# Performance work log

Measured on AMD Instinct MI355X. Metric: run time of the kernel, lower is better.

The kernel has to match this reference:

```python
import jax, jax.numpy as jnp
from jax import lax
import numpy as np

VOCAB, EMBED, HIDDEN, MEL = 256, 256, 1024, 80


def lstm_seq(x_seq, Wih, Whh, bih, bhh):
    """x_seq: [T, B, in]; returns hidden sequence [T, B, H]. PyTorch gate order i,f,g,o."""
    H = Whh.shape[1]
    B = x_seq.shape[1]
    b = bih + bhh

    def step(carry, x):
        h, c = carry
        g = x @ Wih.T + h @ Whh.T + b  # [B, 4H]
        i, f, gg, o = jnp.split(g, 4, axis=-1)
        c = jax.nn.sigmoid(f) * c + jax.nn.sigmoid(i) * jnp.tanh(gg)
        h = jax.nn.sigmoid(o) * jnp.tanh(c)
        return (h, c), h

    init = (jnp.zeros((B, H), x_seq.dtype), jnp.zeros((B, H), x_seq.dtype))
    _, ys = lax.scan(step, init, x_seq)
    return ys


def setup_inputs() -> dict:
    key = jax.random.key(0)
    ks = jax.random.split(key, 13)
    s_h = 1.0 / np.sqrt(HIDDEN)
    u = lambda k, shape, s: jax.random.uniform(k, shape, jnp.float32, -s, s)
    return {
        "text": jax.random.randint(ks[0], (64, 1024), 0, VOCAB),
        "text_lens": jax.random.randint(ks[1], (64,), 1, 1024),
        "max_audio_len": 1000,
        "W_emb": jax.random.normal(ks[2], (VOCAB, EMBED), jnp.float32),
        "enc_Wih": u(ks[3], (4 * HIDDEN, EMBED), s_h),
        "enc_Whh": u(ks[4], (4 * HIDDEN, HIDDEN), s_h),
        "enc_bih": u(ks[5], (4 * HIDDEN,), s_h),
        "enc_bhh": u(ks[6], (4 * HIDDEN,), s_h),
        "dec_Wih": u(ks[7], (4 * HIDDEN, MEL), s_h),
        "dec_Whh": u(ks[8], (4 * HIDDEN, HIDDEN), s_h),
        "dec_bih": u(ks[9], (4 * HIDDEN,), s_h),
        "dec_bhh": u(ks[10], (4 * HIDDEN,), s_h),
        "lin_W": u(ks[11], (MEL, HIDDEN), s_h),
        "lin_b": u(ks[12], (MEL,), s_h),
    }


def reference(text, text_lens, max_audio_len, W_emb, enc_Wih, enc_Whh, enc_bih,
              enc_bhh, dec_Wih, dec_Whh, dec_bih, dec_bhh, lin_W, lin_b):
    B = text.shape[0]
    # Encoder over text (output unused downstream, but computed as in the original).
    emb = W_emb[text]                      # [B, T, E]
    enc_out = lstm_seq(emb.transpose(1, 0, 2), enc_Wih, enc_Whh, enc_bih, enc_bhh)
    enc_out = enc_out.transpose(1, 0, 2)   # [B, T, H]

    b_dec = dec_bih + dec_bhh

    def dec_step(carry, _):
        h, c, x = carry                    # x: [B, MEL] previous frame
        g = x @ dec_Wih.T + h @ dec_Whh.T + b_dec
        i, f, gg, o = jnp.split(g, 4, axis=-1)
        c = jax.nn.sigmoid(f) * c + jax.nn.sigmoid(i) * jnp.tanh(gg)
        h = jax.nn.sigmoid(o) * jnp.tanh(c)
        frame = h @ lin_W.T + lin_b        # [B, MEL]
        return (h, c, frame), frame

    init = (jnp.zeros((B, HIDDEN), jnp.float32),
            jnp.zeros((B, HIDDEN), jnp.float32),
            jnp.zeros((B, MEL), jnp.float32))
    _, frames = lax.scan(dec_step, init, None, length=max_audio_len)
    return frames.transpose(1, 0, 2)       # [B, max_audio_len, MEL]
```

## Files before the change

kernel.cpp:

```cpp
#include <hip/hip_runtime.h>
#include <math.h>

#define HIDDEN 1024
#define MEL    80
#define TSTEPS 1000
#define BATCH  64

#define NBLK 64
#define TPB  1024

typedef unsigned long long ull;

__device__ __forceinline__ float sigm_f(float x) { return 1.0f / (1.0f + __expf(-x)); }
__device__ __forceinline__ float tanh_f(float x) { return 1.0f - 2.0f / (1.0f + __expf(2.0f * x)); }

__global__ __launch_bounds__(TPB, 4) void tts_recur(
    const float* __restrict__ dec_Wih,
    const float* __restrict__ dec_Whh,
    const float* __restrict__ dec_bih,
    const float* __restrict__ dec_bhh,
    const float* __restrict__ lin_W,
    const float* __restrict__ lin_b,
    float* __restrict__ h_hist,
    ull* __restrict__ hbuf)
{
    const int tid  = threadIdx.x;
    const int blk  = blockIdx.x;
    const int wv   = tid >> 6;
    const int lane = tid & 63;
    const int jj   = lane & 15;
    const int gate = lane >> 4;
    const int unit_g = blk * 16 + jj;
    const int row_g  = gate * HIDDEN + unit_g;

    if (wv == 0) __builtin_amdgcn_s_setprio(3);

    __shared__ __align__(16) float hEx[16][64];
    __shared__ float part[2][64 * 17];

    const float* wih = dec_Wih + (size_t)row_g * MEL;
    const float* whh = dec_Whh + (size_t)row_g * HIDDEN + wv * 64;
    float4 w[16];
#pragma unroll
    for (int k = 0; k < 16; ++k)
        w[k] = *(const float4*)(whh + k * 4);
#pragma unroll 1
    for (int m = 0; m < MEL; ++m) {
        const float aw = wih[m];
        const float4* lw4 = (const float4*)(lin_W + (size_t)m * HIDDEN + wv * 64);
#pragma unroll
        for (int k = 0; k < 8; ++k) {
            const float4 lw = lw4[k];
            w[k].x = fmaf(aw, lw.x, w[k].x); w[k].y = fmaf(aw, lw.y, w[k].y);
            w[k].z = fmaf(aw, lw.z, w[k].z); w[k].w = fmaf(aw, lw.w, w[k].w);
        }
#pragma unroll
        for (int k = 8; k < 16; ++k) {
            const float4 lw = lw4[k];
            w[k].x = fmaf(aw, lw.x, w[k].x); w[k].y = fmaf(aw, lw.y, w[k].y);
            w[k].z = fmaf(aw, lw.z, w[k].z); w[k].w = fmaf(aw, lw.w, w[k].w);
        }
    }
    float b_comb_r = dec_bih[row_g] + dec_bhh[row_g];
    const float b_dec_r = b_comb_r;
    for (int m = 0; m < MEL; ++m)
        b_comb_r = fmaf(wih[m], lin_b[m], b_comb_r);

    float c_prev = 0.0f;

    if (wv == 0) {
        const float g = b_dec_r;
        const float gi = __shfl(g, jj, 64);
        const float gg = __shfl(g, 32 + jj, 64);
        const float go = __shfl(g, 48 + jj, 64);
        const float c  = sigm_f(gi) * tanh_f(gg);
        const float h  = sigm_f(go) * tanh_f(c);
        c_prev = c;
        if (lane < 16) {
            const ull pk = ((ull)1u << 32) | (ull)__float_as_uint(h);
            __hip_atomic_store(hbuf + unit_g, pk,
                               __ATOMIC_RELAXED, __HIP_MEMORY_SCOPE_SYSTEM);
            h_hist[unit_g] = h;
        }
    }

    for (int t = 1; t < TSTEPS; ++t) {
        const int buf = t & 1;
        {
            const ull* src = hbuf + ((t - 1) & 1) * HIDDEN;
            ull v = __hip_atomic_load(src + tid, __ATOMIC_RELAXED, __HIP_MEMORY_SCOPE_SYSTEM);
            while ((unsigned)(v >> 32) != (unsigned)t)
                v = __hip_atomic_load(src + tid, __ATOMIC_RELAXED, __HIP_MEMORY_SCOPE_SYSTEM);
            hEx[wv][lane] = __uint_as_float((unsigned)v);
        }
        __builtin_amdgcn_wave_barrier();

        const float4* hp = (const float4*)&hEx[wv][0];
        float a0 = 0.f, a1 = 0.f, a2 = 0.f, a3 = 0.f;
#pragma unroll
        for (int k = 0; k < 16; k += 4) {
            const float4 h0 = hp[k], h1 = hp[k + 1], h2 = hp[k + 2], h3 = hp[k + 3];
            a0 = fmaf(w[k].x, h0.x, a0);   a0 = fmaf(w[k].y, h0.y, a0);
            a0 = fmaf(w[k].z, h0.z, a0);   a0 = fmaf(w[k].w, h0.w, a0);
            a1 = fmaf(w[k+1].x, h1.x, a1); a1 = fmaf(w[k+1].y, h1.y, a1);
            a1 = fmaf(w[k+1].z, h1.z, a1); a1 = fmaf(w[k+1].w, h1.w, a1);
            a2 = fmaf(w[k+2].x, h2.x, a2); a2 = fmaf(w[k+2].y, h2.y, a2);
            a2 = fmaf(w[k+2].z, h2.z, a2); a2 = fmaf(w[k+2].w, h2.w, a2);
            a3 = fmaf(w[k+3].x, h3.x, a3); a3 = fmaf(w[k+3].y, h3.y, a3);
            a3 = fmaf(w[k+3].z, h3.z, a3); a3 = fmaf(w[k+3].w, h3.w, a3);
        }
        part[buf][lane * 17 + wv] = (a0 + a1) + (a2 + a3);
        __syncthreads();

        if (wv == 0) {
            const float* pr = &part[buf][lane * 17];
            float p[16];
#pragma unroll
            for (int i = 0; i < 16; ++i) p[i] = pr[i];
            const float s = (((p[0]+p[1])+(p[2]+p[3])) + ((p[4]+p[5])+(p[6]+p[7])))
                          + (((p[8]+p[9])+(p[10]+p[11])) + ((p[12]+p[13])+(p[14]+p[15])));
            const float g = s + b_comb_r;
            const float gi = __shfl(g, jj, 64);
            const float gf = __shfl(g, 16 + jj, 64);
            const float gg = __shfl(g, 32 + jj, 64);
            const float go = __shfl(g, 48 + jj, 64);
            const float c  = sigm_f(gf) * c_prev + sigm_f(gi) * tanh_f(gg);
            const float h  = sigm_f(go) * tanh_f(c);
            c_prev = c;
            if (lane < 16) {
                const ull pk = ((ull)(unsigned)(t + 1) << 32) | (ull)__float_as_uint(h);
                __hip_atomic_store(hbuf + buf * HIDDEN + unit_g, pk,
                                   __ATOMIC_RELAXED, __HIP_MEMORY_SCOPE_SYSTEM);
                h_hist[(size_t)t * HIDDEN + unit_g] = h;
            }
        }
    }
}

__global__ __launch_bounds__(128) void tts_frames(
    const float* __restrict__ lin_W, const float* __restrict__ lin_b,
    const float* __restrict__ h_hist, float* __restrict__ out)
{
    const int t = blockIdx.x;
    const int tid = threadIdx.x;
    __shared__ __align__(16) float h_sh[HIDDEN];
    __shared__ float f_s[MEL];
    const float4* src = (const float4*)(h_hist + (size_t)t * HIDDEN);
    ((float4*)h_sh)[tid] = src[tid];
    ((float4*)h_sh)[tid + 128] = src[tid + 128];
    __syncthreads();
    if (tid < MEL) {
        const float* wrow = lin_W + (size_t)tid * HIDDEN;
        float acc = lin_b[tid];
#pragma unroll 8
        for (int c = 0; c < HIDDEN; ++c)
            acc = fmaf(wrow[c], h_sh[c], acc);
        f_s[tid] = acc;
    }
    __syncthreads();
    for (int idx = tid; idx < BATCH * MEL; idx += 128) {
        const int b = idx / MEL;
        const int m = idx - b * MEL;
        out[(size_t)b * TSTEPS * MEL + (size_t)t * MEL + m] = f_s[m];
    }
}

extern "C" void kernel_launch(void* const* d_in, const int* in_sizes, int n_in,
                              void* d_out, int out_size, void* d_ws, size_t ws_size,
                              hipStream_t stream) {
    const float* dec_Wih = (const float*)d_in[8];
    const float* dec_Whh = (const float*)d_in[9];
    const float* dec_bih = (const float*)d_in[10];
    const float* dec_bhh = (const float*)d_in[11];
    const float* lin_W   = (const float*)d_in[12];
    const float* lin_b   = (const float*)d_in[13];
    float* out = (float*)d_out;

    float* h_hist = (float*)d_ws;
    ull* hbuf = (ull*)((char*)d_ws + (size_t)TSTEPS * HIDDEN * sizeof(float));

    hipLaunchKernelGGL(tts_recur, dim3(NBLK), dim3(TPB), 0, stream,
                       dec_Wih, dec_Whh, dec_bih, dec_bhh, lin_W, lin_b, h_hist, hbuf);
    hipLaunchKernelGGL(tts_frames, dim3(TSTEPS), dim3(128), 0, stream,
                       lin_W, lin_b, h_hist, out);
}
```

Baseline: 2.187 ms.

## Map one hidden unit per wave to drop block barrier in LSTM recurrence

The persistent recurrent kernel is reorganized so that each wave owns one hidden unit, with its 64 lanes covering 4 gates times 16 column chunks. The cross-wave shared-memory partial sum and __syncthreads are replaced by a shuffle-xor reduction inside the wave. Every wave now reads the full h vector itself, issuing 16 tagged atomic loads per lane into padded LDS. The grid changes to 256 blocks of 256 threads, and atomic scope is narrowed from system to agent. The aim is to remove block-level synchronization and the serial reduction on the per-step critical path, at the cost of 4x more global polling traffic per step.

Measured after the change: 8.702 ms. +297.9%, slower.

```diff
diff --git a/kernel.cpp b/kernel.cpp
--- a/kernel.cpp
+++ b/kernel.cpp
@@ -6,15 +6,17 @@
 #define TSTEPS 1000
 #define BATCH  64
 
-#define NBLK 64
-#define TPB  1024
+#define NBLK 256
+#define TPB  256
 
 typedef unsigned long long ull;
 
 __device__ __forceinline__ float sigm_f(float x) { return 1.0f / (1.0f + __expf(-x)); }
 __device__ __forceinline__ float tanh_f(float x) { return 1.0f - 2.0f / (1.0f + __expf(2.0f * x)); }
 
-__global__ __launch_bounds__(TPB, 4) void tts_recur(
+#define HEXP 1088
+
+__global__ __launch_bounds__(TPB, 1) void tts_recur(
     const float* __restrict__ dec_Wih,
     const float* __restrict__ dec_Whh,
     const float* __restrict__ dec_bih,
@@ -25,21 +27,17 @@
     ull* __restrict__ hbuf)
 {
     const int tid  = threadIdx.x;
-    const int blk  = blockIdx.x;
     const int wv   = tid >> 6;
     const int lane = tid & 63;
-    const int jj   = lane & 15;
     const int gate = lane >> 4;
-    const int unit_g = blk * 16 + jj;
-    const int row_g  = gate * HIDDEN + unit_g;
+    const int c    = lane & 15;
+    const int u    = blockIdx.x * 4 + wv;
+    const int row_g = gate * HIDDEN + u;
 
-    if (wv == 0) __builtin_amdgcn_s_setprio(3);
-
-    __shared__ __align__(16) float hEx[16][64];
-    __shared__ float part[2][64 * 17];
+    __shared__ __align__(16) float hEx[4][HEXP];
 
     const float* wih = dec_Wih + (size_t)row_g * MEL;
-    const float* whh = dec_Whh + (size_t)row_g * HIDDEN + wv * 64;
+    const float* whh = dec_Whh + (size_t)row_g * HIDDEN + c * 64;
     float4 w[16];
 #pragma unroll
     for (int k = 0; k < 16; ++k)
@@ -47,7 +45,7 @@
 #pragma unroll 1
     for (int m = 0; m < MEL; ++m) {
         const float aw = wih[m];
-        const float4* lw4 = (const float4*)(lin_W + (size_t)m * HIDDEN + wv * 64);
+        const float4* lw4 = (const float4*)(lin_W + (size_t)m * HIDDEN + c * 64);
 #pragma unroll
         for (int k = 0; k < 8; ++k) {
             const float4 lw = lw4[k];
@@ -68,34 +66,43 @@
 
     float c_prev = 0.0f;
 
-    if (wv == 0) {
+    {
         const float g = b_dec_r;
-        const float gi = __shfl(g, jj, 64);
-        const float gg = __shfl(g, 32 + jj, 64);
-        const float go = __shfl(g, 48 + jj, 64);
-        const float c  = sigm_f(gi) * tanh_f(gg);
-        const float h  = sigm_f(go) * tanh_f(c);
-        c_prev = c;
-        if (lane < 16) {
+        const float gi = __shfl(g, c, 64);
+        const float gf = __shfl(g, 16 + c, 64);
+        const float gg = __shfl(g, 32 + c, 64);
+        const float go = __shfl(g, 48 + c, 64);
+        const float cc = sigm_f(gf) * c_prev + sigm_f(gi) * tanh_f(gg);
+        const float h  = sigm_f(go) * tanh_f(cc);
+        c_prev = cc;
+        if (lane == 0) {
             const ull pk = ((ull)1u << 32) | (ull)__float_as_uint(h);
-            __hip_atomic_store(hbuf + unit_g, pk,
-                               __ATOMIC_RELAXED, __HIP_MEMORY_SCOPE_SYSTEM);
-            h_hist[unit_g] = h;
+            __hip_atomic_store(hbuf + u, pk,
+                               __ATOMIC_RELAXED, __HIP_MEMORY_SCOPE_AGENT);
+            h_hist[u] = h;
         }
     }
 
     for (int t = 1; t < TSTEPS; ++t) {
-        const int buf = t & 1;
+        const unsigned tag = (unsigned)t;
         {
             const ull* src = hbuf + ((t - 1) & 1) * HIDDEN;
-            ull v = __hip_atomic_load(src + tid, __ATOMIC_RELAXED, __HIP_MEMORY_SCOPE_SYSTEM);
-            while ((unsigned)(v >> 32) != (unsigned)t)
-                v = __hip_atomic_load(src + tid, __ATOMIC_RELAXED, __HIP_MEMORY_SCOPE_SYSTEM);
-            hEx[wv][lane] = __uint_as_float((unsigned)v);
+            ull v[16];
+#pragma unroll
+            for (int j = 0; j < 16; ++j)
+                v[j] = __hip_atomic_load(src + lane + 64 * j,
+                                         __ATOMIC_RELAXED, __HIP_MEMORY_SCOPE_AGENT);
+#pragma unroll
+            for (int j = 0; j < 16; ++j) {
+                while ((unsigned)(v[j] >> 32) != tag)
+                    v[j] = __hip_atomic_load(src + lane + 64 * j,
+                                             __ATOMIC_RELAXED, __HIP_MEMORY_SCOPE_AGENT);
+                hEx[wv][lane + 68 * j] = __uint_as_float((unsigned)v[j]);
+            }
         }
         __builtin_amdgcn_wave_barrier();
 
-        const float4* hp = (const float4*)&hEx[wv][0];
+        const float4* hp = (const float4*)(&hEx[wv][68 * c]);
         float a0 = 0.f, a1 = 0.f, a2 = 0.f, a3 = 0.f;
 #pragma unroll
         for (int k = 0; k < 16; k += 4) {
@@ -109,30 +116,25 @@
             a3 = fmaf(w[k+3].x, h3.x, a3); a3 = fmaf(w[k+3].y, h3.y, a3);
             a3 = fmaf(w[k+3].z, h3.z, a3); a3 = fmaf(w[k+3].w, h3.w, a3);
         }
-        part[buf][lane * 17 + wv] = (a0 + a1) + (a2 + a3);
-        __syncthreads();
+        float acc = (a0 + a1) + (a2 + a3);
+        acc += __shfl_xor(acc, 1, 64);
+        acc += __shfl_xor(acc, 2, 64);
+        acc += __shfl_xor(acc, 4, 64);
+        acc += __shfl_xor(acc, 8, 64);
+        const float g = acc + b_comb_r;
+        const float gi = __shfl(g, c, 64);
+        const float gf = __shfl(g, 16 + c, 64);
+        const float gg = __shfl(g, 32 + c, 64);
+        const float go = __shfl(g, 48 + c, 64);
+        const float cc = sigm_f(gf) * c_prev + sigm_f(gi) * tanh_f(gg);
+        const float h  = sigm_f(go) * tanh_f(cc);
+        c_prev = cc;
 
-        if (wv == 0) {
-            const float* pr = &part[buf][lane * 17];
-            float p[16];
-#pragma unroll
-            for (int i = 0; i < 16; ++i) p[i] = pr[i];
-            const float s = (((p[0]+p[1])+(p[2]+p[3])) + ((p[4]+p[5])+(p[6]+p[7])))
-                          + (((p[8]+p[9])+(p[10]+p[11])) + ((p[12]+p[13])+(p[14]+p[15])));
-            const float g = s + b_comb_r;
-            const float gi = __shfl(g, jj, 64);
-            const float gf = __shfl(g, 16 + jj, 64);
-            const float gg = __shfl(g, 32 + jj, 64);
-            const float go = __shfl(g, 48 + jj, 64);
-            const float c  = sigm_f(gf) * c_prev + sigm_f(gi) * tanh_f(gg);
-            const float h  = sigm_f(go) * tanh_f(c);
-            c_prev = c;
-            if (lane < 16) {
-                const ull pk = ((ull)(unsigned)(t + 1) << 32) | (ull)__float_as_uint(h);
-                __hip_atomic_store(hbuf + buf * HIDDEN + unit_g, pk,
-                                   __ATOMIC_RELAXED, __HIP_MEMORY_SCOPE_SYSTEM);
-                h_hist[(size_t)t * HIDDEN + unit_g] = h;
-            }
+        if (lane == 0) {
+            const ull pk = ((ull)(unsigned)(t + 1) << 32) | (ull)__float_as_uint(h);
+            __hip_atomic_store(hbuf + (t & 1) * HIDDEN + u, pk,
+                               __ATOMIC_RELAXED, __HIP_MEMORY_SCOPE_AGENT);
+            h_hist[(size_t)t * HIDDEN + u] = h;
         }
     }
 }
@@ -153,8 +155,8 @@
         const float* wrow = lin_W + (size_t)tid * HIDDEN;
         float acc = lin_b[tid];
 #pragma unroll 8
-        for (int c = 0; c < HIDDEN; ++c)
-            acc = fmaf(wrow[c], h_sh[c], acc);
+        for (int cc = 0; cc < HIDDEN; ++cc)
+            acc = fmaf(wrow[cc], h_sh[cc], acc);
         f_s[tid] = acc;
     }
     __syncthreads();
```

## Spread LSTM cell update across all waves and use agent-scope atomics

Applied to the files above, without the earlier changes.

The per-step gate reduction and cell update move from wave 0 alone to all 16 waves. Each wave reads 16 partials for its own hidden unit, reduces them with xor shuffles, and computes the cell for that one unit. Inter-block h exchange now uses agent-scope atomics instead of system scope, and the wave-0 priority boost is removed. This aims to cut the serial tail on the recurrence critical path and lower atomic coherence cost. In exchange every wave does redundant transcendental work, and the reduction order changes slightly.

After: 3.874 ms. 77.1% more time.

```diff
diff --git a/kernel.cpp b/kernel.cpp
--- a/kernel.cpp
+++ b/kernel.cpp
@@ -30,10 +30,7 @@
     const int lane = tid & 63;
     const int jj   = lane & 15;
     const int gate = lane >> 4;
-    const int unit_g = blk * 16 + jj;
-    const int row_g  = gate * HIDDEN + unit_g;
-
-    if (wv == 0) __builtin_amdgcn_s_setprio(3);
+    const int row_g  = gate * HIDDEN + blk * 16 + jj;
 
     __shared__ __align__(16) float hEx[16][64];
     __shared__ float part[2][64 * 17];
@@ -66,21 +63,21 @@
     for (int m = 0; m < MEL; ++m)
         b_comb_r = fmaf(wih[m], lin_b[m], b_comb_r);
 
-    float c_prev = 0.0f;
+    float c_prev;
 
-    if (wv == 0) {
-        const float g = b_dec_r;
-        const float gi = __shfl(g, jj, 64);
-        const float gg = __shfl(g, 32 + jj, 64);
-        const float go = __shfl(g, 48 + jj, 64);
+    {
+        const float bdw = __shfl(b_dec_r, (lane & 48) + wv, 64);
+        const float gi = __shfl(bdw, 0, 64);
+        const float gg = __shfl(bdw, 32, 64);
+        const float go = __shfl(bdw, 48, 64);
         const float c  = sigm_f(gi) * tanh_f(gg);
         const float h  = sigm_f(go) * tanh_f(c);
         c_prev = c;
-        if (lane < 16) {
+        if (lane == 0) {
             const ull pk = ((ull)1u << 32) | (ull)__float_as_uint(h);
-            __hip_atomic_store(hbuf + unit_g, pk,
-                               __ATOMIC_RELAXED, __HIP_MEMORY_SCOPE_SYSTEM);
-            h_hist[unit_g] = h;
+            __hip_atomic_store(hbuf + blk * 16 + wv, pk,
+                               __ATOMIC_RELAXED, __HIP_MEMORY_SCOPE_AGENT);
+            h_hist[blk * 16 + wv] = h;
         }
     }
 
@@ -88,9 +85,9 @@
         const int buf = t & 1;
         {
             const ull* src = hbuf + ((t - 1) & 1) * HIDDEN;
-            ull v = __hip_atomic_load(src + tid, __ATOMIC_RELAXED, __HIP_MEMORY_SCOPE_SYSTEM);
+            ull v = __hip_atomic_load(src + tid, __ATOMIC_RELAXED, __HIP_MEMORY_SCOPE_AGENT);
             while ((unsigned)(v >> 32) != (unsigned)t)
-                v = __hip_atomic_load(src + tid, __ATOMIC_RELAXED, __HIP_MEMORY_SCOPE_SYSTEM);
+                v = __hip_atomic_load(src + tid, __ATOMIC_RELAXED, __HIP_MEMORY_SCOPE_AGENT);
             hEx[wv][lane] = __uint_as_float((unsigned)v);
         }
         __builtin_amdgcn_wave_barrier();
@@ -112,26 +109,25 @@
         part[buf][lane * 17 + wv] = (a0 + a1) + (a2 + a3);
         __syncthreads();
 
-        if (wv == 0) {
-            const float* pr = &part[buf][lane * 17];
-            float p[16];
-#pragma unroll
-            for (int i = 0; i < 16; ++i) p[i] = pr[i];
-            const float s = (((p[0]+p[1])+(p[2]+p[3])) + ((p[4]+p[5])+(p[6]+p[7])))
-                          + (((p[8]+p[9])+(p[10]+p[11])) + ((p[12]+p[13])+(p[14]+p[15])));
-            const float g = s + b_comb_r;
-            const float gi = __shfl(g, jj, 64);
-            const float gf = __shfl(g, 16 + jj, 64);
-            const float gg = __shfl(g, 32 + jj, 64);
-            const float go = __shfl(g, 48 + jj, 64);
+        {
+            float s = part[buf][((lane & 48) + wv) * 17 + (lane & 15)];
+            s += __shfl_xor(s, 1, 64);
+            s += __shfl_xor(s, 2, 64);
+            s += __shfl_xor(s, 4, 64);
+            s += __shfl_xor(s, 8, 64);
+            const float gpre = s + __shfl(b_comb_r, (lane & 48) + wv, 64);
+            const float gi = __shfl(gpre, 0, 64);
+            const float gf = __shfl(gpre, 16, 64);
+            const float gg = __shfl(gpre, 32, 64);
+            const float go = __shfl(gpre, 48, 64);
             const float c  = sigm_f(gf) * c_prev + sigm_f(gi) * tanh_f(gg);
             const float h  = sigm_f(go) * tanh_f(c);
             c_prev = c;
-            if (lane < 16) {
+            if (lane == 0) {
                 const ull pk = ((ull)(unsigned)(t + 1) << 32) | (ull)__float_as_uint(h);
-                __hip_atomic_store(hbuf + buf * HIDDEN + unit_g, pk,
-                                   __ATOMIC_RELAXED, __HIP_MEMORY_SCOPE_SYSTEM);
-                h_hist[(size_t)t * HIDDEN + unit_g] = h;
+                __hip_atomic_store(hbuf + buf * HIDDEN + blk * 16 + wv, pk,
+                                   __ATOMIC_RELAXED, __HIP_MEMORY_SCOPE_AGENT);
+                h_hist[(size_t)t * HIDDEN + blk * 16 + wv] = h;
             }
         }
     }
@@ -153,8 +149,8 @@
         const float* wrow = lin_W + (size_t)tid * HIDDEN;
         float acc = lin_b[tid];
 #pragma unroll 8
-        for (int c = 0; c < HIDDEN; ++c)
-            acc = fmaf(wrow[c], h_sh[c], acc);
+        for (int cc = 0; cc < HIDDEN; ++cc)
+            acc = fmaf(wrow[cc], h_sh[cc], acc);
         f_s[tid] = acc;
     }
     __syncthreads();
```
